# Optimization experiments

Hardware: AMD Instinct MI355X
Metric: run time of the kernel (lower is better)

Reference implementation:

```python
import jax, jax.numpy as jnp
import numpy as np

B, E, T = 16, 64, 1000
DIM, HEADS, NB_F, LAYERS, NUM_CLASSES = 32, 4, 64, 2, 2
BAND_K = 51
DH = DIM // HEADS  # head dim = 8
EPS = 1e-5


def _layernorm(x, g, b):
    mu = jnp.mean(x, axis=-1, keepdims=True)
    var = jnp.var(x, axis=-1, keepdims=True)
    return (x - mu) * jax.lax.rsqrt(var + EPS) * g + b


def setup_inputs() -> dict:
    key = jax.random.key(0)
    ks = jax.random.split(key, 24)
    d = {}
    d['x'] = jax.random.normal(ks[0], (B, 1, E, T), dtype=jnp.float32)
    # fixed band-pass filters, stacked as one conv: [4 out, 1 in, 1, 51]
    d['band_w'] = jax.random.normal(ks[1], (4, 1, 1, BAND_K), dtype=jnp.float32) * 0.1
    d['pw_w'] = jax.random.normal(ks[2], (DIM, 4), dtype=jnp.float32) * 0.5
    d['bn_g'] = jnp.ones((DIM,), jnp.float32)
    d['bn_b'] = jnp.zeros((DIM,), jnp.float32)
    d['bn_m'] = jnp.zeros((DIM,), jnp.float32)
    d['bn_v'] = jnp.ones((DIM,), jnp.float32)
    s = 1.0 / np.sqrt(DIM)
    L = LAYERS
    d['ln1_g'] = jnp.ones((L, DIM), jnp.float32)
    d['ln1_b'] = jnp.zeros((L, DIM), jnp.float32)
    d['wqkv'] = jax.random.normal(ks[3], (L, DIM, 3 * DIM), jnp.float32) * s
    d['proj_mat'] = jax.random.normal(ks[4], (L, HEADS, DH, NB_F), jnp.float32)
    d['wproj'] = jax.random.normal(ks[5], (L, DIM, DIM), jnp.float32) * s
    d['bproj'] = jnp.zeros((L, DIM), jnp.float32)
    d['ln2_g'] = jnp.ones((L, DIM), jnp.float32)
    d['ln2_b'] = jnp.zeros((L, DIM), jnp.float32)
    d['w1'] = jax.random.normal(ks[6], (L, DIM, 2 * DIM), jnp.float32) * s
    d['b1'] = jnp.zeros((L, 2 * DIM), jnp.float32)
    d['w2'] = jax.random.normal(ks[7], (L, 2 * DIM, DIM), jnp.float32) * (1.0 / np.sqrt(2 * DIM))
    d['b2'] = jnp.zeros((L, DIM), jnp.float32)
    d['norm_g'] = jnp.ones((DIM,), jnp.float32)
    d['norm_b'] = jnp.zeros((DIM,), jnp.float32)
    d['pool_w'] = jax.random.normal(ks[8], (DIM, 1), jnp.float32) * s
    d['pool_b'] = jnp.zeros((1,), jnp.float32)
    d['fc_w'] = jax.random.normal(ks[9], (DIM, NUM_CLASSES), jnp.float32) * s
    d['fc_b'] = jnp.zeros((NUM_CLASSES,), jnp.float32)
    return d


def _favor(x, pm):
    # x: [B,N,C] -> [B,N,H,F] feature map
    b, n, c = x.shape
    xh = x.reshape(b, n, HEADS, DH)
    p = jnp.einsum('bnhd,hdf->bnhf', xh, pm)
    return jax.nn.elu(p) + 1.0


def _attn(x, wqkv, pm, wproj, bproj):
    b, n, c = x.shape
    qkv = x @ wqkv  # [B,N,3C]
    q, k, v = jnp.split(qkv, 3, axis=-1)
    Q = _favor(q, pm)
    K = _favor(k, pm)
    V = v.reshape(b, n, HEADS, DH)
    # NOTE: faithful to source — KV sums over batch AND sequence
    KV = jnp.einsum('bnhf,bnhd->hfd', K, V)
    Z = 1.0 / jnp.einsum('bnhf,hfd->bnh', Q, KV)
    out = jnp.einsum('bnhf,hfd->bnhd', Q, KV) * Z[..., None]
    return out.reshape(b, n, c) @ wproj + bproj


def _tokenize(x, band_w, pw_w, bn_g, bn_b, bn_m, bn_v):
    pad = BAND_K // 2
    xc = jax.lax.conv_general_dilated(
        x, band_w, window_strides=(1, 1), padding=((0, 0), (pad, pad)),
        dimension_numbers=('NCHW', 'OIHW', 'NCHW'))  # [B,4,E,T]
    h = jnp.einsum('bcet,oc->boet', xc, pw_w)  # 1x1 conv -> [B,DIM,E,T]
    h = (h - bn_m[:, None, None]) * jax.lax.rsqrt(bn_v[:, None, None] + EPS) \
        * bn_g[:, None, None] + bn_b[:, None, None]
    h = jax.nn.gelu(h, approximate=False)
    b, c, e, t = h.shape
    h = h.reshape(b, c, e, t // 4, 4).mean(axis=-1)  # AvgPool (1,4)
    h = h.reshape(b, c, e * (t // 4))
    return jnp.transpose(h, (0, 2, 1))  # [B, N, DIM]


def reference(x, band_w, pw_w, bn_g, bn_b, bn_m, bn_v, ln1_g, ln1_b, wqkv,
              proj_mat, wproj, bproj, ln2_g, ln2_b, w1, b1, w2, b2,
              norm_g, norm_b, pool_w, pool_b, fc_w, fc_b):
    h = _tokenize(x, band_w, pw_w, bn_g, bn_b, bn_m, bn_v)
    for l in range(LAYERS):
        h = h + _attn(_layernorm(h, ln1_g[l], ln1_b[l]), wqkv[l], proj_mat[l],
                      wproj[l], bproj[l])
        m = _layernorm(h, ln2_g[l], ln2_b[l])
        m = jax.nn.gelu(m @ w1[l] + b1[l], approximate=False) @ w2[l] + b2[l]
        h = h + m
    h = _layernorm(h, norm_g, norm_b)
    w = jax.nn.softmax(h @ pool_w + pool_b, axis=1)  # [B,N,1]
    pooled = jnp.sum(w * h, axis=1)  # [B,DIM]
    return pooled @ fc_w + fc_b
```

## Files before the change

kernel.cpp:

```cpp
#include <hip/hip_runtime.h>
#include <math.h>

#define NTOK   256000
#define TOKB   16000
#define EPS    1e-5f

__device__ __forceinline__ float gelu_f(float x){
  return 0.5f*x*(1.0f+erff(x*0.70710678118654752440f));
}
__device__ __forceinline__ float elu1_f(float x){
  return x>0.0f ? x+1.0f : __expf(x);
}

__global__ __launch_bounds__(256) void k_prep(
    const float* __restrict__ proj_mat, const float* __restrict__ w1,
    float* __restrict__ pmT, float* __restrict__ w1T)
{
  const int i = blockIdx.x*256 + threadIdx.x;
  if (i < 4096){
    const int l=i>>11, h=(i>>9)&3, f=(i>>3)&63, d=i&7;
    pmT[i] = proj_mat[l*2048 + h*512 + d*64 + f];
    const int j=(i>>5)&63, i2=i&31;
    w1T[i] = w1[l*2048 + i2*64 + j];
  }
}

__global__ __launch_bounds__(256) void k_tokenize(
    const float* __restrict__ x, const float* __restrict__ band_w,
    const float* __restrict__ pw_w, const float* __restrict__ bn_g,
    const float* __restrict__ bn_b, const float* __restrict__ bn_m,
    const float* __restrict__ bn_v, float* __restrict__ hout)
{
  __shared__ float sx[1050];
  __shared__ float sbw[4][51];
  __shared__ float spw[32][4];
  __shared__ float sscale[32], sshift[32];
  const int tid = threadIdx.x;
  const int b = blockIdx.x >> 6, e = blockIdx.x & 63;
  const float* xr = x + (size_t)(b*64 + e)*1000;
  for (int i=tid;i<1050;i+=256){ int t=i-25; sx[i]=(t>=0&&t<1000)?xr[t]:0.0f; }
  for (int i=tid;i<204;i+=256){ sbw[i/51][i%51] = band_w[i]; }
  for (int i=tid;i<128;i+=256){ spw[i>>2][i&3] = pw_w[i]; }
  if (tid<32){ float sc = bn_g[tid]*rsqrtf(bn_v[tid]+EPS);
               sscale[tid]=sc; sshift[tid]=bn_b[tid]-bn_m[tid]*sc; }
  __syncthreads();
  const int tp = tid;
  if (tp < 250) {
    float acc[32];
    #pragma unroll
    for (int o=0;o<32;o++) acc[o]=0.0f;
    for (int j=0;j<4;j++){
      const int t = 4*tp+j;
      float c0=0,c1=0,c2=0,c3=0;
      for (int k=0;k<51;k++){
        float xv = sx[t+k];
        c0 += xv*sbw[0][k]; c1 += xv*sbw[1][k];
        c2 += xv*sbw[2][k]; c3 += xv*sbw[3][k];
      }
      #pragma unroll
      for (int o=0;o<32;o++){
        float hv = spw[o][0]*c0 + spw[o][1]*c1 + spw[o][2]*c2 + spw[o][3]*c3;
        hv = hv*sscale[o] + sshift[o];
        acc[o] += gelu_f(hv);
      }
    }
    const int tok = b*TOKB + e*250 + tp;
    float4* dst = (float4*)(hout + (size_t)tok*32);
    #pragma unroll
    for (int o8=0;o8<8;o8++)
      dst[o8] = make_float4(acc[o8*4]*0.25f, acc[o8*4+1]*0.25f,
                            acc[o8*4+2]*0.25f, acc[o8*4+3]*0.25f);
  }
}

__global__ __launch_bounds__(256) void k_kv_partial(
    const float* __restrict__ hbuf, const float* __restrict__ lg,
    const float* __restrict__ lb, const float* __restrict__ W,
    const float* __restrict__ pm,
    float* __restrict__ kvpart)
{
  __shared__ __align__(16) float sk[128][36];
  __shared__ __align__(16) float sv[128][36];
  const int tid = threadIdx.x;
  {
    const int tloc = tid & 127, half = tid >> 7;
    const int tok = blockIdx.x*128 + tloc;
    float hx[32];
    const float4* src = (const float4*)(hbuf + (size_t)tok*32);
    #pragma unroll
    for (int i=0;i<8;i++){ float4 v4=src[i]; hx[4*i]=v4.x; hx[4*i+1]=v4.y; hx[4*i+2]=v4.z; hx[4*i+3]=v4.w; }
    float mu=0;
    #pragma unroll
    for (int i=0;i<32;i++) mu += hx[i];
    mu *= (1.0f/32.0f);
    float vs=0;
    #pragma unroll
    for (int i=0;i<32;i++){ float d=hx[i]-mu; vs += d*d; }
    const float inv = rsqrtf(vs*(1.0f/32.0f)+EPS);
    float xn[32];
    #pragma unroll
    for (int i=0;i<32;i++) xn[i] = (hx[i]-mu)*inv*lg[i]+lb[i];
    const int j0 = half*16;
    float ka[16], va[16];
    #pragma unroll
    for (int jj=0;jj<16;jj++){ ka[jj]=0.0f; va[jj]=0.0f; }
    #pragma unroll
    for (int i=0;i<32;i++){
      const float* rk = W + i*96 + 32 + j0;
      const float* rv = W + i*96 + 64 + j0;
      #pragma unroll
      for (int jj=0;jj<16;jj++){ ka[jj] += xn[i]*rk[jj]; va[jj] += xn[i]*rv[jj]; }
    }
    float4* skp = (float4*)&sk[tloc][j0];
    float4* svp = (float4*)&sv[tloc][j0];
    #pragma unroll
    for (int q4=0;q4<4;q4++){
      skp[q4] = make_float4(ka[4*q4],ka[4*q4+1],ka[4*q4+2],ka[4*q4+3]);
      svp[q4] = make_float4(va[4*q4],va[4*q4+1],va[4*q4+2],va[4*q4+3]);
    }
  }
  __syncthreads();
  const int hh = tid>>6, f = tid&63;
  float pm0,pm1,pm2,pm3,pm4,pm5,pm6,pm7;
  {
    const float* pmp = pm + (size_t)hh*512 + f;
    pm0=pmp[0]; pm1=pmp[64]; pm2=pmp[128]; pm3=pmp[192];
    pm4=pmp[256]; pm5=pmp[320]; pm6=pmp[384]; pm7=pmp[448];
  }
  float a0=0,a1=0,a2=0,a3=0,a4=0,a5=0,a6=0,a7=0;
  #pragma unroll 4
  for (int t=0;t<128;t++){
    const float4* k4 = (const float4*)&sk[t][hh*8];
    const float4* v4 = (const float4*)&sv[t][hh*8];
    float4 ka = k4[0], kb = k4[1];
    float kd = ka.x*pm0 + ka.y*pm1 + ka.z*pm2 + ka.w*pm3
             + kb.x*pm4 + kb.y*pm5 + kb.z*pm6 + kb.w*pm7;
    const float Kf = elu1_f(kd);
    float4 va = v4[0], vb = v4[1];
    a0 += Kf*va.x; a1 += Kf*va.y; a2 += Kf*va.z; a3 += Kf*va.w;
    a4 += Kf*vb.x; a5 += Kf*vb.y; a6 += Kf*vb.z; a7 += Kf*vb.w;
  }
  float4* dst = (float4*)(kvpart + (size_t)blockIdx.x*2048 + tid*8);
  dst[0] = make_float4(a0,a1,a2,a3);
  dst[1] = make_float4(a4,a5,a6,a7);
}

__global__ __launch_bounds__(256) void k_kv_reduce1(
    const float* __restrict__ kvpart, float* __restrict__ p2)
{
  const int chunk = blockIdx.x >> 3;
  const int e = (blockIdx.x&7)*256 + threadIdx.x;
  float acc=0.0f;
  const int base = chunk*200;
  for (int ab=0; ab<200; ab++) acc += kvpart[(size_t)(base+ab)*2048 + e];
  p2[chunk*2048 + e] = acc;
}

__global__ __launch_bounds__(256) void k_kv_reduce2(
    const float* __restrict__ p2, float* __restrict__ KV)
{
  const int hf = threadIdx.x;
  float acc[8];
  #pragma unroll
  for (int d=0;d<8;d++) acc[d]=0.0f;
  for (int c=0;c<10;c++){
    #pragma unroll
    for (int d=0;d<8;d++) acc[d] += p2[c*2048 + hf*8 + d];
  }
  #pragma unroll
  for (int d=0;d<8;d++) KV[hf*8+d]=acc[d];
}

__global__ __launch_bounds__(256) void k_attn(
    float* __restrict__ hbuf,
    const float* __restrict__ lg, const float* __restrict__ lb,
    const float* __restrict__ wq,
    const float* __restrict__ pmT,
    const float* __restrict__ wp,
    const float* __restrict__ bp,
    const float* __restrict__ KV)
{
  const int tok = blockIdx.x*256 + threadIdx.x;
  float4* hp = (float4*)(hbuf + (size_t)tok*32);

  float xn[32];
  {
    float hx[32];
    #pragma unroll
    for (int i=0;i<8;i++){ float4 v=hp[i]; hx[4*i]=v.x; hx[4*i+1]=v.y; hx[4*i+2]=v.z; hx[4*i+3]=v.w; }
    float mu=0;
    #pragma unroll
    for (int i=0;i<32;i++) mu += hx[i];
    mu *= (1.0f/32.0f);
    float vs=0;
    #pragma unroll
    for (int i=0;i<32;i++){ float d=hx[i]-mu; vs += d*d; }
    const float inv = rsqrtf(vs*(1.0f/32.0f)+EPS);
    #pragma unroll
    for (int i=0;i<32;i++) xn[i] = (hx[i]-mu)*inv*lg[i]+lb[i];
  }

  float q[32];
  #pragma unroll
  for (int j=0;j<32;j++) q[j]=0.0f;
  #pragma unroll
  for (int i=0;i<32;i++){
    const float* r = wq + i*96;
    #pragma unroll
    for (int j=0;j<32;j++) q[j] += xn[i]*r[j];
  }

  #pragma unroll
  for (int hh=0;hh<4;hh++){
    float ao[8];
    #pragma unroll
    for (int d=0;d<8;d++) ao[d]=0.0f;
    #pragma unroll 4
    for (int f=0;f<64;f++){
      const float* pm8 = pmT + hh*512 + f*8;
      float qd = q[hh*8+0]*pm8[0] + q[hh*8+1]*pm8[1] + q[hh*8+2]*pm8[2] + q[hh*8+3]*pm8[3]
               + q[hh*8+4]*pm8[4] + q[hh*8+5]*pm8[5] + q[hh*8+6]*pm8[6] + q[hh*8+7]*pm8[7];
      const float Qf = elu1_f(qd);
      const float* kv8 = KV + hh*512 + f*8;
      ao[0] += Qf*kv8[0]; ao[1] += Qf*kv8[1]; ao[2] += Qf*kv8[2]; ao[3] += Qf*kv8[3];
      ao[4] += Qf*kv8[4]; ao[5] += Qf*kv8[5]; ao[6] += Qf*kv8[6]; ao[7] += Qf*kv8[7];
    }
    const float den = ao[0]+ao[1]+ao[2]+ao[3]+ao[4]+ao[5]+ao[6]+ao[7];
    const float z = 1.0f/den;
    #pragma unroll
    for (int d=0;d<8;d++) q[hh*8+d] = ao[d]*z;
  }

  float p[32];
  #pragma unroll
  for (int o=0;o<32;o++) p[o] = bp[o];
  #pragma unroll
  for (int i=0;i<32;i++){
    const float* r = wp + i*32;
    #pragma unroll
    for (int o=0;o<32;o++) p[o] += q[i]*r[o];
  }
  #pragma unroll
  for (int o4=0;o4<8;o4++){
    float4 hx4 = hp[o4];
    hp[o4] = make_float4(hx4.x+p[4*o4+0], hx4.y+p[4*o4+1],
                         hx4.z+p[4*o4+2], hx4.w+p[4*o4+3]);
  }
}

__global__ __launch_bounds__(256) void k_ffn(
    float* __restrict__ hbuf,
    const float* __restrict__ lg, const float* __restrict__ lb,
    const float* __restrict__ w1T,
    const float* __restrict__ b1,
    const float* __restrict__ w2,
    const float* __restrict__ b2)
{
  const int tok = blockIdx.x*256 + threadIdx.x;
  float4* hp = (float4*)(hbuf + (size_t)tok*32);

  float m[32];
  {
    float hx[32];
    #pragma unroll
    for (int i=0;i<8;i++){ float4 v=hp[i]; hx[4*i]=v.x; hx[4*i+1]=v.y; hx[4*i+2]=v.z; hx[4*i+3]=v.w; }
    float mu=0;
    #pragma unroll
    for (int i=0;i<32;i++) mu += hx[i];
    mu *= (1.0f/32.0f);
    float vs=0;
    #pragma unroll
    for (int i=0;i<32;i++){ float d=hx[i]-mu; vs += d*d; }
    const float inv = rsqrtf(vs*(1.0f/32.0f)+EPS);
    #pragma unroll
    for (int i=0;i<32;i++) m[i] = (hx[i]-mu)*inv*lg[i]+lb[i];
  }

  float f[32];
  #pragma unroll
  for (int c=0;c<32;c++) f[c] = b2[c];

  #pragma unroll 4
  for (int j=0;j<64;j++){
    const float* r1 = w1T + j*32;
    float g = b1[j];
    #pragma unroll
    for (int i=0;i<32;i++) g += m[i]*r1[i];
    const float gg = gelu_f(g);
    const float* r2 = w2 + j*32;
    #pragma unroll
    for (int c=0;c<32;c++) f[c] += gg*r2[c];
  }

  #pragma unroll
  for (int o4=0;o4<8;o4++){
    float4 hx4 = hp[o4];
    hp[o4] = make_float4(hx4.x+f[4*o4+0], hx4.y+f[4*o4+1],
                         hx4.z+f[4*o4+2], hx4.w+f[4*o4+3]);
  }
}

__global__ __launch_bounds__(256) void k_pool_score(
    const float* __restrict__ hbuf, const float* __restrict__ ng,
    const float* __restrict__ nb, const float* __restrict__ pw,
    const float* __restrict__ pb, float* __restrict__ s)
{
  const int tok = blockIdx.x*256 + threadIdx.x;
  float hx[32];
  const float4* src = (const float4*)(hbuf + (size_t)tok*32);
  #pragma unroll
  for (int i=0;i<8;i++){ float4 v4=src[i]; hx[4*i]=v4.x; hx[4*i+1]=v4.y; hx[4*i+2]=v4.z; hx[4*i+3]=v4.w; }
  float mu=0;
  #pragma unroll
  for (int i=0;i<32;i++) mu += hx[i];
  mu *= (1.0f/32.0f);
  float vs=0;
  #pragma unroll
  for (int i=0;i<32;i++){ float d=hx[i]-mu; vs += d*d; }
  const float inv = rsqrtf(vs*(1.0f/32.0f)+EPS);
  float sv = pb[0];
  #pragma unroll
  for (int i=0;i<32;i++) sv += ((hx[i]-mu)*inv*ng[i]+nb[i])*pw[i];
  s[tok]=sv;
}

__global__ __launch_bounds__(256) void k_softmax_stats(
    const float* __restrict__ s, float* __restrict__ bmax, float* __restrict__ bsum)
{
  __shared__ float red[256];
  __shared__ float smax_sh;
  const int b = blockIdx.x, tid = threadIdx.x;
  const float* sbp = s + (size_t)b*TOKB;
  float mx = -INFINITY;
  for (int i=tid;i<TOKB;i+=256) mx = fmaxf(mx, sbp[i]);
  red[tid]=mx; __syncthreads();
  for (int st=128;st>0;st>>=1){ if(tid<st) red[tid]=fmaxf(red[tid],red[tid+st]); __syncthreads(); }
  if (tid==0) smax_sh = red[0];
  __syncthreads();
  const float smax = smax_sh;
  float acc=0.0f;
  for (int i=tid;i<TOKB;i+=256) acc += __expf(sbp[i]-smax);
  __syncthreads();
  red[tid]=acc; __syncthreads();
  for (int st=128;st>0;st>>=1){ if(tid<st) red[tid]+=red[tid+st]; __syncthreads(); }
  if (tid==0){ bmax[b]=smax; bsum[b]=red[0]; }
}

__global__ __launch_bounds__(256) void k_pool_partial(
    const float* __restrict__ hbuf, const float* __restrict__ ng,
    const float* __restrict__ nb, const float* __restrict__ s,
    const float* __restrict__ bmax, float* __restrict__ pp)
{
  __shared__ float red[256][33];
  const int b = blockIdx.x/63, ch = blockIdx.x%63;
  const int tid = threadIdx.x;
  const int n = ch*256+tid;
  if (n < TOKB) {
    const int tok = b*TOKB+n;
    float hx[32];
    const float4* src = (const float4*)(hbuf + (size_t)tok*32);
    #pragma unroll
    for (int i=0;i<8;i++){ float4 v4=src[i]; hx[4*i]=v4.x; hx[4*i+1]=v4.y; hx[4*i+2]=v4.z; hx[4*i+3]=v4.w; }
    float mu=0;
    #pragma unroll
    for (int i=0;i<32;i++) mu += hx[i];
    mu *= (1.0f/32.0f);
    float vs=0;
    #pragma unroll
    for (int i=0;i<32;i++){ float d=hx[i]-mu; vs += d*d; }
    const float inv = rsqrtf(vs*(1.0f/32.0f)+EPS);
    const float w = __expf(s[tok]-bmax[b]);
    #pragma unroll
    for (int i=0;i<32;i++) red[tid][i] = w*((hx[i]-mu)*inv*ng[i]+nb[i]);
  } else {
    #pragma unroll
    for (int i=0;i<32;i++) red[tid][i]=0.0f;
  }
  __syncthreads();
  if (tid<32){
    float acc=0.0f;
    for (int t=0;t<256;t++) acc += red[t][tid];
    pp[(size_t)blockIdx.x*32 + tid] = acc;
  }
}

__global__ __launch_bounds__(64) void k_pool_final(
    const float* __restrict__ pp, const float* __restrict__ bsum,
    const float* __restrict__ fcw, const float* __restrict__ fcb,
    float* __restrict__ out)
{
  __shared__ float sp[32];
  const int b = blockIdx.x, tid = threadIdx.x;
  if (tid<32){
    float acc=0.0f;
    for (int ch=0;ch<63;ch++) acc += pp[(size_t)(b*63+ch)*32+tid];
    sp[tid] = acc / bsum[b];
  }
  __syncthreads();
  if (tid<2){
    float v = fcb[tid];
    for (int o=0;o<32;o++) v += sp[o]*fcw[o*2+tid];
    out[b*2+tid]=v;
  }
}

extern "C" void kernel_launch(void* const* d_in, const int* in_sizes, int n_in,
                              void* d_out, int out_size, void* d_ws, size_t ws_size,
                              hipStream_t stream)
{
  const float* x      = (const float*)d_in[0];
  const float* band_w = (const float*)d_in[1];
  const float* pw_w   = (const float*)d_in[2];
  const float* bn_g   = (const float*)d_in[3];
  const float* bn_b   = (const float*)d_in[4];
  const float* bn_m   = (const float*)d_in[5];
  const float* bn_v   = (const float*)d_in[6];
  const float* ln1_g  = (const float*)d_in[7];
  const float* ln1_b  = (const float*)d_in[8];
  const float* wqkv   = (const float*)d_in[9];
  const float* proj   = (const float*)d_in[10];
  const float* wproj  = (const float*)d_in[11];
  const float* bprojp = (const float*)d_in[12];
  const float* ln2_g  = (const float*)d_in[13];
  const float* ln2_b  = (const float*)d_in[14];
  const float* w1     = (const float*)d_in[15];
  const float* b1     = (const float*)d_in[16];
  const float* w2     = (const float*)d_in[17];
  const float* b2     = (const float*)d_in[18];
  const float* norm_g = (const float*)d_in[19];
  const float* norm_b = (const float*)d_in[20];
  const float* pool_w = (const float*)d_in[21];
  const float* pool_b = (const float*)d_in[22];
  const float* fc_w   = (const float*)d_in[23];
  const float* fc_b   = (const float*)d_in[24];
  float* out = (float*)d_out;
  float* ws  = (float*)d_ws;

  float* hbuf  = ws;
  float* kvp   = hbuf + 8192000;
  float* p2    = kvp  + 4096000;
  float* KV    = p2   + 20480;
  float* pmT   = KV   + 2048;
  float* w1T   = pmT  + 4096;
  float* sbuf  = w1T  + 4096;
  float* bmax  = sbuf + 256000;
  float* bsum  = bmax + 16;
  float* pp    = bsum + 16;

  k_prep<<<16,256,0,stream>>>(proj, w1, pmT, w1T);
  k_tokenize<<<1024,256,0,stream>>>(x, band_w, pw_w, bn_g, bn_b, bn_m, bn_v, hbuf);
  for (int l=0;l<2;l++){
    k_kv_partial<<<2000,256,0,stream>>>(hbuf, ln1_g+l*32, ln1_b+l*32,
                                        wqkv+l*3072, proj+l*2048, kvp);
    k_kv_reduce1<<<80,256,0,stream>>>(kvp, p2);
    k_kv_reduce2<<<1,256,0,stream>>>(p2, KV);
    k_attn<<<1000,256,0,stream>>>(hbuf, ln1_g+l*32, ln1_b+l*32,
                                  wqkv+l*3072, pmT+l*2048,
                                  wproj+l*1024, bprojp+l*32, KV);
    k_ffn<<<1000,256,0,stream>>>(hbuf, ln2_g+l*32, ln2_b+l*32,
                                 w1T+l*2048, b1+l*64, w2+l*2048, b2+l*32);
  }
  k_pool_score<<<1000,256,0,stream>>>(hbuf, norm_g, norm_b, pool_w, pool_b, sbuf);
  k_softmax_stats<<<16,256,0,stream>>>(sbuf, bmax, bsum);
  k_pool_partial<<<16*63,256,0,stream>>>(hbuf, norm_g, norm_b, sbuf, bmax, pp);
  k_pool_final<<<16,64,0,stream>>>(pp, bsum, fc_w, fc_b, out);
}
```

Before: 729.3 us.

## Broadcast weights via readlane and LDS instead of per-thread scalar global loads

The kv_partial, attn and ffn kernels stop reading the small weight matrices through per-thread scalar or global loads. Weights are staged transposed in shared memory and read as float4, or held one row per lane in registers and broadcast with amdgcn readlane inside the f/j/t loops. In kv_partial each token is split across two adjacent threads, and the K/V tiles are read from LDS once into registers, then broadcast with readlane. This aims to cut the cost of loading weights, at the price of many readlane instructions (scalar-pipe pressure) and more registers.

After: 881.0 us. +20.8%, slower.

```diff
diff --git a/kernel.cpp b/kernel.cpp
--- a/kernel.cpp
+++ b/kernel.cpp
@@ -10,6 +10,9 @@
 }
 __device__ __forceinline__ float elu1_f(float x){
   return x>0.0f ? x+1.0f : __expf(x);
+}
+__device__ __forceinline__ float rl(float x, int l){
+  return __int_as_float(__builtin_amdgcn_readlane(__float_as_int(x), l));
 }
 
 __global__ __launch_bounds__(256) void k_prep(
@@ -81,9 +84,15 @@
 {
   __shared__ __align__(16) float sk[128][36];
   __shared__ __align__(16) float sv[128][36];
+  __shared__ __align__(16) float swkT[64][32];
   const int tid = threadIdx.x;
+  for (int idx=tid;idx<2048;idx+=256){
+    int i = idx&31, j = idx>>5;
+    swkT[j][i] = W[i*96 + 32 + j];
+  }
+  __syncthreads();
   {
-    const int tloc = tid & 127, half = tid >> 7;
+    const int tloc = tid>>1, half = tid&1;
     const int tok = blockIdx.x*128 + tloc;
     float hx[32];
     const float4* src = (const float4*)(hbuf + (size_t)tok*32);
@@ -101,22 +110,19 @@
     #pragma unroll
     for (int i=0;i<32;i++) xn[i] = (hx[i]-mu)*inv*lg[i]+lb[i];
     const int j0 = half*16;
-    float ka[16], va[16];
-    #pragma unroll
-    for (int jj=0;jj<16;jj++){ ka[jj]=0.0f; va[jj]=0.0f; }
-    #pragma unroll
-    for (int i=0;i<32;i++){
-      const float* rk = W + i*96 + 32 + j0;
-      const float* rv = W + i*96 + 64 + j0;
+    #pragma unroll 4
+    for (int jj=0;jj<16;jj++){
+      const int j = j0+jj;
+      const float4* wk4 = (const float4*)&swkT[j][0];
+      const float4* wv4 = (const float4*)&swkT[32+j][0];
+      float ka=0, va=0;
       #pragma unroll
-      for (int jj=0;jj<16;jj++){ ka[jj] += xn[i]*rk[jj]; va[jj] += xn[i]*rv[jj]; }
-    }
-    float4* skp = (float4*)&sk[tloc][j0];
-    float4* svp = (float4*)&sv[tloc][j0];
-    #pragma unroll
-    for (int q4=0;q4<4;q4++){
-      skp[q4] = make_float4(ka[4*q4],ka[4*q4+1],ka[4*q4+2],ka[4*q4+3]);
-      svp[q4] = make_float4(va[4*q4],va[4*q4+1],va[4*q4+2],va[4*q4+3]);
+      for (int i4=0;i4<8;i4++){
+        float4 wk = wk4[i4], wv = wv4[i4];
+        ka += xn[4*i4+0]*wk.x + xn[4*i4+1]*wk.y + xn[4*i4+2]*wk.z + xn[4*i4+3]*wk.w;
+        va += xn[4*i4+0]*wv.x + xn[4*i4+1]*wv.y + xn[4*i4+2]*wv.z + xn[4*i4+3]*wv.w;
+      }
+      sk[tloc][j]=ka; sv[tloc][j]=va;
     }
   }
   __syncthreads();
@@ -127,18 +133,29 @@
     pm0=pmp[0]; pm1=pmp[64]; pm2=pmp[128]; pm3=pmp[192];
     pm4=pmp[256]; pm5=pmp[320]; pm6=pmp[384]; pm7=pmp[448];
   }
+  float4 kA0,kB0,kA1,kB1,vA0,vB0,vA1,vB1;
+  {
+    const float4* p0 = (const float4*)&sk[f][hh*8];       kA0=p0[0]; kB0=p0[1];
+    const float4* p1 = (const float4*)&sk[64+f][hh*8];    kA1=p1[0]; kB1=p1[1];
+    const float4* p2 = (const float4*)&sv[f][hh*8];       vA0=p2[0]; vB0=p2[1];
+    const float4* p3 = (const float4*)&sv[64+f][hh*8];    vA1=p3[0]; vB1=p3[1];
+  }
   float a0=0,a1=0,a2=0,a3=0,a4=0,a5=0,a6=0,a7=0;
-  #pragma unroll 4
-  for (int t=0;t<128;t++){
-    const float4* k4 = (const float4*)&sk[t][hh*8];
-    const float4* v4 = (const float4*)&sv[t][hh*8];
-    float4 ka = k4[0], kb = k4[1];
-    float kd = ka.x*pm0 + ka.y*pm1 + ka.z*pm2 + ka.w*pm3
-             + kb.x*pm4 + kb.y*pm5 + kb.z*pm6 + kb.w*pm7;
+  #pragma unroll 2
+  for (int t=0;t<64;t++){
+    float kd = rl(kA0.x,t)*pm0 + rl(kA0.y,t)*pm1 + rl(kA0.z,t)*pm2 + rl(kA0.w,t)*pm3
+             + rl(kB0.x,t)*pm4 + rl(kB0.y,t)*pm5 + rl(kB0.z,t)*pm6 + rl(kB0.w,t)*pm7;
     const float Kf = elu1_f(kd);
-    float4 va = v4[0], vb = v4[1];
-    a0 += Kf*va.x; a1 += Kf*va.y; a2 += Kf*va.z; a3 += Kf*va.w;
-    a4 += Kf*vb.x; a5 += Kf*vb.y; a6 += Kf*vb.z; a7 += Kf*vb.w;
+    a0 += Kf*rl(vA0.x,t); a1 += Kf*rl(vA0.y,t); a2 += Kf*rl(vA0.z,t); a3 += Kf*rl(vA0.w,t);
+    a4 += Kf*rl(vB0.x,t); a5 += Kf*rl(vB0.y,t); a6 += Kf*rl(vB0.z,t); a7 += Kf*rl(vB0.w,t);
+  }
+  #pragma unroll 2
+  for (int t=0;t<64;t++){
+    float kd = rl(kA1.x,t)*pm0 + rl(kA1.y,t)*pm1 + rl(kA1.z,t)*pm2 + rl(kA1.w,t)*pm3
+             + rl(kB1.x,t)*pm4 + rl(kB1.y,t)*pm5 + rl(kB1.z,t)*pm6 + rl(kB1.w,t)*pm7;
+    const float Kf = elu1_f(kd);
+    a0 += Kf*rl(vA1.x,t); a1 += Kf*rl(vA1.y,t); a2 += Kf*rl(vA1.z,t); a3 += Kf*rl(vA1.w,t);
+    a4 += Kf*rl(vB1.x,t); a5 += Kf*rl(vB1.y,t); a6 += Kf*rl(vB1.z,t); a7 += Kf*rl(vB1.w,t);
   }
   float4* dst = (float4*)(kvpart + (size_t)blockIdx.x*2048 + tid*8);
   dst[0] = make_float4(a0,a1,a2,a3);
@@ -180,7 +197,20 @@
     const float* __restrict__ bp,
     const float* __restrict__ KV)
 {
-  const int tok = blockIdx.x*256 + threadIdx.x;
+  __shared__ __align__(16) float swqT[32][32];
+  __shared__ __align__(16) float swpT[32][32];
+  __shared__ float s1g[32], s1b[32], sbp[32];
+  const int tid = threadIdx.x;
+  for (int idx=tid; idx<1024; idx+=256){
+    int j=idx>>5, i=idx&31;
+    swqT[j][i] = wq[i*96+j];
+    swpT[j][i] = wp[i*32+j];
+  }
+  if (tid<32){ s1g[tid]=lg[tid]; s1b[tid]=lb[tid]; sbp[tid]=bp[tid]; }
+  __syncthreads();
+
+  const int lane = tid & 63;
+  const int tok = blockIdx.x*256 + tid;
   float4* hp = (float4*)(hbuf + (size_t)tok*32);
 
   float xn[32];
@@ -197,54 +227,60 @@
     for (int i=0;i<32;i++){ float d=hx[i]-mu; vs += d*d; }
     const float inv = rsqrtf(vs*(1.0f/32.0f)+EPS);
     #pragma unroll
-    for (int i=0;i<32;i++) xn[i] = (hx[i]-mu)*inv*lg[i]+lb[i];
-  }
-
-  float q[32];
-  #pragma unroll
-  for (int j=0;j<32;j++) q[j]=0.0f;
-  #pragma unroll
-  for (int i=0;i<32;i++){
-    const float* r = wq + i*96;
-    #pragma unroll
-    for (int j=0;j<32;j++) q[j] += xn[i]*r[j];
-  }
-
+    for (int i=0;i<32;i++) xn[i] = (hx[i]-mu)*inv*s1g[i]+s1b[i];
+  }
+
+  float att[32];
   #pragma unroll
   for (int hh=0;hh<4;hh++){
-    float ao[8];
-    #pragma unroll
-    for (int d=0;d<8;d++) ao[d]=0.0f;
+    float qh[8];
+    #pragma unroll
+    for (int d=0;d<8;d++){
+      const float4* wr = (const float4*)&swqT[hh*8+d][0];
+      float a=0;
+      #pragma unroll
+      for (int i4=0;i4<8;i4++){
+        float4 w = wr[i4];
+        a += xn[4*i4+0]*w.x + xn[4*i4+1]*w.y + xn[4*i4+2]*w.z + xn[4*i4+3]*w.w;
+      }
+      qh[d]=a;
+    }
+    const float4* pmb = (const float4*)(pmT + hh*512 + lane*8);
+    float4 pA = pmb[0], pB = pmb[1];
+    const float4* kvb = (const float4*)(KV + hh*512 + lane*8);
+    float4 kA = kvb[0], kB = kvb[1];
+    float a0=0,a1=0,a2=0,a3=0,a4=0,a5=0,a6=0,a7=0;
     #pragma unroll 4
-    for (int f=0;f<64;f++){
-      const float* pm8 = pmT + hh*512 + f*8;
-      float qd = q[hh*8+0]*pm8[0] + q[hh*8+1]*pm8[1] + q[hh*8+2]*pm8[2] + q[hh*8+3]*pm8[3]
-               + q[hh*8+4]*pm8[4] + q[hh*8+5]*pm8[5] + q[hh*8+6]*pm8[6] + q[hh*8+7]*pm8[7];
+    for (int f=0; f<64; f++){
+      float qd = qh[0]*rl(pA.x,f)+qh[1]*rl(pA.y,f)+qh[2]*rl(pA.z,f)+qh[3]*rl(pA.w,f)
+               + qh[4]*rl(pB.x,f)+qh[5]*rl(pB.y,f)+qh[6]*rl(pB.z,f)+qh[7]*rl(pB.w,f);
       const float Qf = elu1_f(qd);
-      const float* kv8 = KV + hh*512 + f*8;
-      ao[0] += Qf*kv8[0]; ao[1] += Qf*kv8[1]; ao[2] += Qf*kv8[2]; ao[3] += Qf*kv8[3];
-      ao[4] += Qf*kv8[4]; ao[5] += Qf*kv8[5]; ao[6] += Qf*kv8[6]; ao[7] += Qf*kv8[7];
+      a0+=Qf*rl(kA.x,f); a1+=Qf*rl(kA.y,f); a2+=Qf*rl(kA.z,f); a3+=Qf*rl(kA.w,f);
+      a4+=Qf*rl(kB.x,f); a5+=Qf*rl(kB.y,f); a6+=Qf*rl(kB.z,f); a7+=Qf*rl(kB.w,f);
     }
-    const float den = ao[0]+ao[1]+ao[2]+ao[3]+ao[4]+ao[5]+ao[6]+ao[7];
+    const float den = a0+a1+a2+a3+a4+a5+a6+a7;
     const float z = 1.0f/den;
-    #pragma unroll
-    for (int d=0;d<8;d++) q[hh*8+d] = ao[d]*z;
-  }
-
-  float p[32];
-  #pragma unroll
-  for (int o=0;o<32;o++) p[o] = bp[o];
-  #pragma unroll
-  for (int i=0;i<32;i++){
-    const float* r = wp + i*32;
-    #pragma unroll
-    for (int o=0;o<32;o++) p[o] += q[i]*r[o];
-  }
+    att[hh*8+0]=a0*z; att[hh*8+1]=a1*z; att[hh*8+2]=a2*z; att[hh*8+3]=a3*z;
+    att[hh*8+4]=a4*z; att[hh*8+5]=a5*z; att[hh*8+6]=a6*z; att[hh*8+7]=a7*z;
+  }
+
   #pragma unroll
   for (int o4=0;o4<8;o4++){
+    float p0=sbp[4*o4+0], p1=sbp[4*o4+1], p2=sbp[4*o4+2], p3=sbp[4*o4+3];
+    const float4* w0 = (const float4*)&swpT[o4*4+0][0];
+    const float4* w1r= (const float4*)&swpT[o4*4+1][0];
+    const float4* w2r= (const float4*)&swpT[o4*4+2][0];
+    const float4* w3 = (const float4*)&swpT[o4*4+3][0];
+    #pragma unroll
+    for (int i4=0;i4<8;i4++){
+      float4 b0=w0[i4], b1=w1r[i4], b2=w2r[i4], b3=w3[i4];
+      p0 += att[4*i4+0]*b0.x + att[4*i4+1]*b0.y + att[4*i4+2]*b0.z + att[4*i4+3]*b0.w;
+      p1 += att[4*i4+0]*b1.x + att[4*i4+1]*b1.y + att[4*i4+2]*b1.z + att[4*i4+3]*b1.w;
+      p2 += att[4*i4+0]*b2.x + att[4*i4+1]*b2.y + att[4*i4+2]*b2.z + att[4*i4+3]*b2.w;
+      p3 += att[4*i4+0]*b3.x + att[4*i4+1]*b3.y + att[4*i4+2]*b3.z + att[4*i4+3]*b3.w;
+    }
     float4 hx4 = hp[o4];
-    hp[o4] = make_float4(hx4.x+p[4*o4+0], hx4.y+p[4*o4+1],
-                         hx4.z+p[4*o4+2], hx4.w+p[4*o4+3]);
+    hp[o4] = make_float4(hx4.x+p0, hx4.y+p1, hx4.z+p2, hx4.w+p3);
   }
 }
 
@@ -256,8 +292,22 @@
     const float* __restrict__ w2,
     const float* __restrict__ b2)
 {
-  const int tok = blockIdx.x*256 + threadIdx.x;
+  const int tid = threadIdx.x;
+  const int lane = tid & 63;
+  const int tok = blockIdx.x*256 + tid;
   float4* hp = (float4*)(hbuf + (size_t)tok*32);
+
+  float W1r[32], W2r[32];
+  {
+    const float4* r1 = (const float4*)(w1T + lane*32);
+    const float4* r2 = (const float4*)(w2  + lane*32);
+    #pragma unroll
+    for (int k=0;k<8;k++){
+      float4 a=r1[k]; W1r[4*k]=a.x; W1r[4*k+1]=a.y; W1r[4*k+2]=a.z; W1r[4*k+3]=a.w;
+      float4 b=r2[k]; W2r[4*k]=b.x; W2r[4*k+1]=b.y; W2r[4*k+2]=b.z; W2r[4*k+3]=b.w;
+    }
+  }
+  const float myb1 = b1[lane];
 
   float m[32];
   {
@@ -280,16 +330,14 @@
   #pragma unroll
   for (int c=0;c<32;c++) f[c] = b2[c];
 
-  #pragma unroll 4
+  #pragma unroll 2
   for (int j=0;j<64;j++){
-    const float* r1 = w1T + j*32;
-    float g = b1[j];
-    #pragma unroll
-    for (int i=0;i<32;i++) g += m[i]*r1[i];
+    float g = rl(myb1, j);
+    #pragma unroll
+    for (int i=0;i<32;i++) g += m[i]*rl(W1r[i], j);
     const float gg = gelu_f(g);
-    const float* r2 = w2 + j*32;
-    #pragma unroll
-    for (int c=0;c<32;c++) f[c] += gg*r2[c];
+    #pragma unroll
+    for (int c=0;c<32;c++) f[c] += gg*rl(W2r[c], j);
   }
 
   #pragma unroll
```
